# Kernel optimization log

Hardware: AMD Instinct MI355X
Metric: run time of the kernel (lower is better)

The kernel has to match this reference:

```python
import jax, jax.numpy as jnp
import numpy as np

LN_EPS = 1e-5


def layer_norm(x, w, b):
    mu = jnp.mean(x, axis=-1, keepdims=True)
    var = jnp.mean(jnp.square(x - mu), axis=-1, keepdims=True)
    return (x - mu) * jax.lax.rsqrt(var + LN_EPS) * w + b


def setup_inputs() -> dict:
    key = jax.random.key(0)
    ks = jax.random.split(key, 10)
    B, S, D, H, DH, F = 2, 2048, 1024, 16, 64, 4096

    def xavier(k, shape):
        fan_in, fan_out = shape[-1], int(np.prod(shape[:-1]))
        lim = float(np.sqrt(6.0 / (fan_in + fan_out)))
        return jax.random.uniform(k, shape, jnp.float32, -lim, lim)

    x = jax.random.normal(ks[0], (B, S, D), jnp.float32)
    W_Q = xavier(ks[1], (H, DH, D))
    W_K = xavier(ks[2], (H, DH, D))
    W_V = xavier(ks[3], (H, DH, D))
    W_O = xavier(ks[4], (D, DH, H))
    mlp_w1 = jax.random.normal(ks[5], (F, D), jnp.float32) * (1.0 / np.sqrt(D))
    mlp_b1 = jnp.zeros((F,), jnp.float32)
    mlp_w2 = jax.random.normal(ks[6], (D, F), jnp.float32) * (1.0 / np.sqrt(F))
    mlp_b2 = jnp.zeros((D,), jnp.float32)
    ln_att_w = jnp.ones((D,), jnp.float32)
    ln_att_b = jnp.zeros((D,), jnp.float32)
    ln_mlp_w = jnp.ones((D,), jnp.float32)
    ln_mlp_b = jnp.zeros((D,), jnp.float32)
    return dict(x=x, W_Q=W_Q, W_K=W_K, W_V=W_V, W_O=W_O,
                ln_att_w=ln_att_w, ln_att_b=ln_att_b,
                ln_mlp_w=ln_mlp_w, ln_mlp_b=ln_mlp_b,
                mlp_w1=mlp_w1, mlp_b1=mlp_b1, mlp_w2=mlp_w2, mlp_b2=mlp_b2)


def reference(x, W_Q, W_K, W_V, W_O, ln_att_w, ln_att_b, ln_mlp_w, ln_mlp_b,
              mlp_w1, mlp_b1, mlp_w2, mlp_b2):
    B, S, D = x.shape
    d_head = W_Q.shape[1]
    y = layer_norm(x, ln_att_w, ln_att_b)
    Q = jnp.einsum('ihd,bpd->biph', W_Q, y)  # [B,H,S,dh]
    K = jnp.einsum('ihd,bpd->biph', W_K, y)
    V = jnp.einsum('ihd,bpd->biph', W_V, y)
    scores = jnp.einsum('biph,biqh->biqp', K, Q)  # [B,H,q,p]
    causal = jnp.tril(jnp.ones((S, S), jnp.bool_))  # True where attended
    masked = scores - 1e10 * (~causal).astype(scores.dtype)
    att = jax.nn.softmax(masked / np.sqrt(d_head), axis=-1)
    z = jnp.einsum('biph,biqp->biqh', V, att)
    x_att = jnp.einsum('dhi,biqh->bqd', W_O, z)
    x = x + x_att
    y2 = layer_norm(x, ln_mlp_w, ln_mlp_b)
    h = jax.nn.relu(y2 @ mlp_w1.T + mlp_b1)
    x = x + (h @ mlp_w2.T + mlp_b2)
    return x, att
```

## Files before the change

### kernel.cpp

```cpp
#include <hip/hip_runtime.h>
#include <hip/hip_bf16.h>
#include <stdint.h>

typedef __attribute__((ext_vector_type(8))) short bf16x8;
typedef __attribute__((ext_vector_type(4))) short short4v;
typedef __attribute__((ext_vector_type(4))) float f32x4;

#define GLOAD16(g, s) __builtin_amdgcn_global_load_lds( \
    (const __attribute__((address_space(1))) void*)(g),  \
    (__attribute__((address_space(3))) void*)(s), 16, 0, 0)

static __device__ __forceinline__ short f2bf(float f) {
  unsigned u = __builtin_bit_cast(unsigned, f);
  u += 0x7fffu + ((u >> 16) & 1u);
  return (short)(u >> 16);
}

static __device__ __forceinline__ f32x4 mfma16(bf16x8 a, bf16x8 b, f32x4 c) {
  return __builtin_amdgcn_mfma_f32_16x16x32_bf16(a, b, c, 0, 0, 0);
}

template <int MODE, int BM, int BN>
static __device__ __forceinline__ void gemm_body(
    int lid, int nbx,
    const short* __restrict__ A, const short* __restrict__ Bw,
    float* __restrict__ outF, short* __restrict__ outB,
    const float* __restrict__ resid, const float* __restrict__ bias,
    int M, int N, int K, short* As, short* Bs) {
  constexpr int RBM = BM / 2, RBN = BN / 2;
  constexpr int FM = RBM / 16, FN = RBN / 16;
  constexpr int TCA = BM / 8, TCB = BN / 8, TC = TCA + TCB;
  const int tid = threadIdx.x, lane = tid & 63, wave = tid >> 6;
  const int m0 = (lid / nbx) * BM, n0 = (lid % nbx) * BN;
  const int wm = (wave & 1) * RBM, wn = (wave >> 1) * RBN;
  const int lr = lane >> 3;
  const int lc = (lane & 7) * 8;
  f32x4 acc[FM][FN] = {};

  for (int kt = 0; kt < K; kt += 64) {
#pragma unroll
    for (int i = 0; i < TC / 4; ++i) {
      const int ch = i * 4 + wave;
      if (ch < TCA) {
        GLOAD16(A + (size_t)(m0 + ch * 8 + lr) * K + kt + lc, &As[ch * 512]);
      } else {
        const int cb = ch - TCA;
        GLOAD16(Bw + (size_t)(n0 + cb * 8 + lr) * K + kt + lc, &Bs[cb * 512]);
      }
    }
    __syncthreads();
#pragma unroll
    for (int kk = 0; kk < 64; kk += 32) {
      bf16x8 af[FM], bfr[FN];
#pragma unroll
      for (int i2 = 0; i2 < FM; ++i2)
        af[i2] = *(const bf16x8*)&As[(wm + i2 * 16 + (lane & 15)) * 64 + kk + (lane >> 4) * 8];
#pragma unroll
      for (int j2 = 0; j2 < FN; ++j2)
        bfr[j2] = *(const bf16x8*)&Bs[(wn + j2 * 16 + (lane & 15)) * 64 + kk + (lane >> 4) * 8];
#pragma unroll
      for (int i2 = 0; i2 < FM; ++i2)
#pragma unroll
        for (int j2 = 0; j2 < FN; ++j2)
          acc[i2][j2] = mfma16(af[i2], bfr[j2], acc[i2][j2]);
    }
    __syncthreads();
  }

#pragma unroll
  for (int i2 = 0; i2 < FM; ++i2)
#pragma unroll
    for (int j2 = 0; j2 < FN; ++j2)
#pragma unroll
      for (int r = 0; r < 4; ++r) {
        const int m = m0 + wm + i2 * 16 + (lane >> 4) * 4 + r;
        const int n = n0 + wn + j2 * 16 + (lane & 15);
        const float v = acc[i2][j2][r];
        if (MODE == 0) {
          const size_t oi = (size_t)(n >> 10) * 4194304 +
              ((size_t)((m >> 11) * 16 + ((n & 1023) >> 6)) * 2048 + (m & 2047)) * 64 +
              (n & 63);
          outB[oi] = f2bf(v);
        } else if (MODE == 1) {
          outF[(size_t)m * N + n] = resid[(size_t)m * N + n] + v;
        } else if (MODE == 2) {
          const float t2 = v + bias[n];
          outB[(size_t)m * N + n] = f2bf(t2 > 0.0f ? t2 : 0.0f);
        } else {
          outF[(size_t)m * N + n] = resid[(size_t)m * N + n] + v + bias[n];
        }
      }
}

template <int MODE, int BM, int BN>
__global__ __launch_bounds__(256) void gemm_bf16k(
    const short* __restrict__ A, const short* __restrict__ Bw,
    float* __restrict__ outF, short* __restrict__ outB,
    const float* __restrict__ resid, const float* __restrict__ bias,
    int M, int N, int K) {
  __shared__ short As[BM * 64];
  __shared__ short Bs[BN * 64];
  const int nbx = gridDim.x, nwg = nbx * gridDim.y;
  int lid = (int)blockIdx.y * nbx + (int)blockIdx.x;
  lid = (lid & 7) * (nwg >> 3) + (lid >> 3);
  gemm_body<MODE, BM, BN>(lid, nbx, A, Bw, outF, outB, resid, bias, M, N, K, As, Bs);
}

__global__ __launch_bounds__(256) void prep_all(
    const float* __restrict__ WQ, const float* __restrict__ WK,
    const float* __restrict__ WV, const float* __restrict__ WO,
    const float* __restrict__ w1, const float* __restrict__ w2,
    const float* __restrict__ x, const float* __restrict__ lnw,
    const float* __restrict__ lnb,
    short* __restrict__ Wqkv, short* __restrict__ Wob,
    short* __restrict__ w1b, short* __restrict__ w2b,
    short* __restrict__ yb) {
  __shared__ float red[8];
  const int bi = blockIdx.x, tid = threadIdx.x;
  if (bi < 3072) {
    const float* src = bi < 1024 ? WQ : (bi < 2048 ? WK : WV);
    const float4 v = ((const float4*)(src + (size_t)(bi & 1023) * 1024))[tid];
    short4v o;
    o[0] = f2bf(v.x); o[1] = f2bf(v.y); o[2] = f2bf(v.z); o[3] = f2bf(v.w);
    ((short4v*)(Wqkv + (size_t)bi * 1024))[tid] = o;
  } else if (bi < 7168) {
    const int i = (bi - 3072) * 256 + tid;
    const float4 v = ((const float4*)w1)[i];
    short4v o;
    o[0] = f2bf(v.x); o[1] = f2bf(v.y); o[2] = f2bf(v.z); o[3] = f2bf(v.w);
    ((short4v*)w1b)[i] = o;
  } else if (bi < 11264) {
    const int i = (bi - 7168) * 256 + tid;
    const float4 v = ((const float4*)w2)[i];
    short4v o;
    o[0] = f2bf(v.x); o[1] = f2bf(v.y); o[2] = f2bf(v.z); o[3] = f2bf(v.w);
    ((short4v*)w2b)[i] = o;
  } else if (bi < 15360) {
    const int idx = (bi - 11264) * 256 + tid;
    const int d = idx >> 10, cc = idx & 1023;
    const int i = cc >> 6, h = cc & 63;
    Wob[idx] = f2bf(WO[((size_t)d * 64 + h) * 16 + i]);
  } else {
    const int row = bi - 15360;
    const int lane = tid & 63, wave = tid >> 6;
    const float4 xv = *(const float4*)&x[(size_t)row * 1024 + tid * 4];
    float s1 = xv.x + xv.y + xv.z + xv.w;
    float s2 = xv.x * xv.x + xv.y * xv.y + xv.z * xv.z + xv.w * xv.w;
#pragma unroll
    for (int off = 1; off < 64; off <<= 1) {
      s1 += __shfl_xor(s1, off);
      s2 += __shfl_xor(s2, off);
    }
    if (lane == 0) { red[wave] = s1; red[4 + wave] = s2; }
    __syncthreads();
    s1 = red[0] + red[1] + red[2] + red[3];
    s2 = red[4] + red[5] + red[6] + red[7];
    const float mu = s1 * (1.0f / 1024.0f);
    const float var = s2 * (1.0f / 1024.0f) - mu * mu;
    const float rs = rsqrtf(var + 1e-5f);
    const float4 wv = *(const float4*)&lnw[tid * 4];
    const float4 bv = *(const float4*)&lnb[tid * 4];
    short4v o;
    o[0] = f2bf((xv.x - mu) * rs * wv.x + bv.x);
    o[1] = f2bf((xv.y - mu) * rs * wv.y + bv.y);
    o[2] = f2bf((xv.z - mu) * rs * wv.z + bv.z);
    o[3] = f2bf((xv.w - mu) * rs * wv.w + bv.w);
    *(short4v*)&yb[(size_t)row * 1024 + tid * 4] = o;
  }
}

__global__ __launch_bounds__(256) void ln_kernel(const float* __restrict__ x,
                                                 const float* __restrict__ w,
                                                 const float* __restrict__ b,
                                                 short* __restrict__ y) {
  const int row = blockIdx.x, tid = threadIdx.x;
  const int lane = tid & 63, wave = tid >> 6;
  const float4 xv = *(const float4*)&x[(size_t)row * 1024 + tid * 4];
  float s1 = xv.x + xv.y + xv.z + xv.w;
  float s2 = xv.x * xv.x + xv.y * xv.y + xv.z * xv.z + xv.w * xv.w;
#pragma unroll
  for (int off = 1; off < 64; off <<= 1) {
    s1 += __shfl_xor(s1, off);
    s2 += __shfl_xor(s2, off);
  }
  __shared__ float red[8];
  if (lane == 0) { red[wave] = s1; red[4 + wave] = s2; }
  __syncthreads();
  s1 = red[0] + red[1] + red[2] + red[3];
  s2 = red[4] + red[5] + red[6] + red[7];
  const float mu = s1 * (1.0f / 1024.0f);
  const float var = s2 * (1.0f / 1024.0f) - mu * mu;
  const float rs = rsqrtf(var + 1e-5f);
  const float4 wv = *(const float4*)&w[tid * 4];
  const float4 bv = *(const float4*)&b[tid * 4];
  short4v o;
  o[0] = f2bf((xv.x - mu) * rs * wv.x + bv.x);
  o[1] = f2bf((xv.y - mu) * rs * wv.y + bv.y);
  o[2] = f2bf((xv.z - mu) * rs * wv.z + bv.z);
  o[3] = f2bf((xv.w - mu) * rs * wv.w + bv.w);
  *(short4v*)&y[(size_t)row * 1024 + tid * 4] = o;
}

__global__ __launch_bounds__(256) void transpose_v(const short* __restrict__ V,
                                                   short* __restrict__ Vt) {
  __shared__ short t[64][72];
  const int bi = blockIdx.y;
  const int p0 = blockIdx.x * 64;
  const short* Vh = V + (size_t)bi * 2048 * 64;
  short* Vth = Vt + (size_t)bi * 64 * 2048;
  const int tid = threadIdx.x;
  {
    const int pr = tid >> 2, h0 = (tid & 3) * 16;
    const bf16x8* src = (const bf16x8*)&Vh[(size_t)(p0 + pr) * 64 + h0];
    bf16x8 v0 = src[0], v1 = src[1];
#pragma unroll
    for (int j = 0; j < 8; ++j) { t[pr][h0 + j] = v0[j]; t[pr][h0 + 8 + j] = v1[j]; }
  }
  __syncthreads();
  {
    const int hr = tid >> 2, pq = (tid & 3) * 16;
    bf16x8 o0, o1;
#pragma unroll
    for (int j = 0; j < 8; ++j) { o0[j] = t[pq + j][hr]; o1[j] = t[pq + 8 + j][hr]; }
    *(bf16x8*)&Vth[(size_t)hr * 2048 + p0 + pq] = o0;
    *(bf16x8*)&Vth[(size_t)hr * 2048 + p0 + pq + 8] = o1;
  }
}

__global__ __launch_bounds__(256, 2) void attn_flash(
    const short* __restrict__ Q, const short* __restrict__ K,
    const short* __restrict__ Vt, float* __restrict__ ml,
    short* __restrict__ zb) {
  __shared__ __align__(16) char smem[34816];
  const int tid = threadIdx.x, lane = tid & 63, pc = tid >> 6;
  const int g = lane >> 4, c = lane & 15;
  const int qt = 63 - (int)blockIdx.x;
  const int bi = blockIdx.y;
  const int b = bi >> 4, hd = bi & 15;
  const size_t hoff = (size_t)bi * 2048 * 64;
  const short* Qh = Q + hoff;
  const short* Kh = K + hoff;
  const short* Vth = Vt + hoff;
  short* zbh = zb + (size_t)b * 2048 * 1024 + hd * 64;

  const int qw = qt * 32;
  const int P = qw + 32;
  const int csz = ((P + 511) >> 9) << 7;
  const int p_lo = pc * csz;
  const int p_hi = min(p_lo + csz, P);

  short* pbuf = (short*)smem + pc * 4224;
  float* mlb  = (float*)(smem + 33792);
  float* zm   = (float*)smem;

  const bf16x8* qp0 = (const bf16x8*)&Qh[(size_t)(qw + c) * 64];
  const bf16x8* qp1 = (const bf16x8*)&Qh[(size_t)(qw + 16 + c) * 64];
  bf16x8 aq[2][2];
  aq[0][0] = qp0[g]; aq[0][1] = qp0[4 + g];
  aq[1][0] = qp1[g]; aq[1][1] = qp1[4 + g];

  float m4[2][4], l4[2][4];
  f32x4 zacc[2][4] = {};
#pragma unroll
  for (int rb = 0; rb < 2; ++rb)
#pragma unroll
    for (int r = 0; r < 4; ++r) { m4[rb][r] = -1e30f; l4[rb][r] = 0.0f; }

  for (int p0 = p_lo; p0 < p_hi; p0 += 128) {
    bf16x8 k0[8], k1[8];
#pragma unroll
    for (int kb = 0; kb < 8; ++kb) {
      int row = p0 + kb * 16 + c;
      row = row < 2047 ? row : 2047;
      const bf16x8* kp = (const bf16x8*)&Kh[(size_t)row * 64];
      k0[kb] = kp[g]; k1[kb] = kp[4 + g];
    }
    const bool needmask = (p0 + 128 > qw);
#pragma unroll
    for (int rb = 0; rb < 2; ++rb) {
      f32x4 s[8];
#pragma unroll
      for (int kb = 0; kb < 8; ++kb) {
        f32x4 z4 = {0.0f, 0.0f, 0.0f, 0.0f};
        z4 = mfma16(aq[rb][0], k0[kb], z4);
        s[kb] = mfma16(aq[rb][1], k1[kb], z4);
      }
#pragma unroll
      for (int r = 0; r < 4; ++r) {
        const int q = qw + rb * 16 + g * 4 + r;
        float v[8];
        if (needmask) {
#pragma unroll
          for (int kb = 0; kb < 8; ++kb)
            v[kb] = (p0 + kb * 16 + c <= q) ? s[kb][r] * 0.125f : -1e30f;
        } else {
#pragma unroll
          for (int kb = 0; kb < 8; ++kb) v[kb] = s[kb][r] * 0.125f;
        }
        float mx = fmaxf(fmaxf(fmaxf(v[0], v[1]), fmaxf(v[2], v[3])),
                         fmaxf(fmaxf(v[4], v[5]), fmaxf(v[6], v[7])));
#pragma unroll
        for (int off = 1; off < 16; off <<= 1)
          mx = fmaxf(mx, __shfl_xor(mx, off));
        const float mn = fmaxf(m4[rb][r], mx);
        const float fac = __expf(m4[rb][r] - mn);
        m4[rb][r] = mn;
        float lsum = 0.0f;
        if (needmask) {
#pragma unroll
          for (int kb = 0; kb < 8; ++kb) {
            const int p = p0 + kb * 16 + c;
            const float e = (p <= q) ? __expf(v[kb] - mn) : 0.0f;
            lsum += e;
            pbuf[(rb * 16 + g * 4 + r) * 132 + kb * 16 + c] = f2bf(e);
          }
        } else {
#pragma unroll
          for (int kb = 0; kb < 8; ++kb) {
            const float e = __expf(v[kb] - mn);
            lsum += e;
            pbuf[(rb * 16 + g * 4 + r) * 132 + kb * 16 + c] = f2bf(e);
          }
        }
        l4[rb][r] = l4[rb][r] * fac + lsum;
#pragma unroll
        for (int hb = 0; hb < 4; ++hb) zacc[rb][hb][r] *= fac;
      }
    }
#pragma unroll
    for (int j = 0; j < 4; ++j) {
      const short4v p0lo = *(const short4v*)&pbuf[c * 132 + j * 32 + g * 8];
      const short4v p0hi = *(const short4v*)&pbuf[c * 132 + j * 32 + g * 8 + 4];
      const short4v p1lo = *(const short4v*)&pbuf[(16 + c) * 132 + j * 32 + g * 8];
      const short4v p1hi = *(const short4v*)&pbuf[(16 + c) * 132 + j * 32 + g * 8 + 4];
      const bf16x8 pa0 = __builtin_shufflevector(p0lo, p0hi, 0, 1, 2, 3, 4, 5, 6, 7);
      const bf16x8 pa1 = __builtin_shufflevector(p1lo, p1hi, 0, 1, 2, 3, 4, 5, 6, 7);
#pragma unroll
      for (int hb = 0; hb < 4; ++hb) {
        const bf16x8 bv =
            *(const bf16x8*)&Vth[(size_t)(hb * 16 + c) * 2048 + p0 + j * 32 + g * 8];
        zacc[0][hb] = mfma16(pa0, bv, zacc[0][hb]);
        zacc[1][hb] = mfma16(pa1, bv, zacc[1][hb]);
      }
    }
  }

#pragma unroll
  for (int rb = 0; rb < 2; ++rb)
#pragma unroll
    for (int r = 0; r < 4; ++r)
#pragma unroll
      for (int off = 1; off < 16; off <<= 1)
        l4[rb][r] += __shfl_xor(l4[rb][r], off);

  if (c == 0) {
#pragma unroll
    for (int rb = 0; rb < 2; ++rb)
#pragma unroll
      for (int r = 0; r < 4; ++r) {
        mlb[(pc * 32 + rb * 16 + g * 4 + r) * 2 + 0] = m4[rb][r];
        mlb[(pc * 32 + rb * 16 + g * 4 + r) * 2 + 1] = l4[rb][r];
      }
  }
  __syncthreads();

  if (pc != 0) {
#pragma unroll
    for (int rb = 0; rb < 2; ++rb)
#pragma unroll
      for (int hb = 0; hb < 4; ++hb)
#pragma unroll
        for (int r = 0; r < 4; ++r)
          zm[((pc - 1) * 32 + rb * 16 + g * 4 + r) * 68 + hb * 16 + c] = zacc[rb][hb][r];
  }
  __syncthreads();
  if (pc == 0) {
#pragma unroll
    for (int rb = 0; rb < 2; ++rb)
#pragma unroll
      for (int r = 0; r < 4; ++r) {
        const int row = rb * 16 + g * 4 + r;
        float M = -1e30f;
#pragma unroll
        for (int j = 0; j < 4; ++j) M = fmaxf(M, mlb[(j * 32 + row) * 2 + 0]);
        float w[4], L = 0.0f;
#pragma unroll
        for (int j = 0; j < 4; ++j) {
          w[j] = __expf(mlb[(j * 32 + row) * 2 + 0] - M);
          L += mlb[(j * 32 + row) * 2 + 1] * w[j];
        }
        const float iL = 1.0f / L;
#pragma unroll
        for (int hb = 0; hb < 4; ++hb) {
          float z = zacc[rb][hb][r] * w[0];
#pragma unroll
          for (int j = 1; j < 4; ++j)
            z += zm[((j - 1) * 32 + row) * 68 + hb * 16 + c] * w[j];
          zbh[(size_t)(qw + row) * 1024 + hb * 16 + c] = f2bf(z * iL);
        }
        if (c == 0)
          ((float2*)ml)[(size_t)bi * 2048 + qw + row] = make_float2(M, iL);
      }
  }
}

__global__ __launch_bounds__(256) void fused_wo_attw(
    const short* __restrict__ zbuf, const short* __restrict__ Wob,
    float* __restrict__ x1, const float* __restrict__ x,
    const short* __restrict__ Q, const short* __restrict__ K,
    const float* __restrict__ ml, float* __restrict__ att) {
  __shared__ __align__(16) char sm[24576];
  if (blockIdx.x < 512) {
    gemm_body<1, 128, 64>((int)blockIdx.x, 16, zbuf, Wob, x1, nullptr, x,
                          nullptr, 4096, 1024, 1024, (short*)sm,
                          (short*)sm + 128 * 64);
    return;
  }
  const int id = (int)blockIdx.x - 512;
  const int bi = id >> 9;
  const int rem = id & 511;
  const int qt = rem >> 3, pt = rem & 7;
  const int tid = threadIdx.x, lane = tid & 63, wave = tid >> 6;
  const int g = lane >> 4, c = lane & 15;
  const int qs = wave >> 1, ph = wave & 1;
  const int qw = qt * 32 + qs * 16;
  const int pb = pt * 256 + ph * 128;
  float* atth = att + (size_t)bi * 2048 * 2048;
  const int r0 = lane >> 3, c4 = (lane & 7) * 4;

  if (pb > qw + 15) {
    const f32x4 zf = {0.0f, 0.0f, 0.0f, 0.0f};
#pragma unroll
    for (int j = 0; j < 4; ++j) {
      __builtin_nontemporal_store(zf, (f32x4*)&atth[(size_t)(qw + r0) * 2048 + pb + j * 32 + c4]);
      __builtin_nontemporal_store(zf, (f32x4*)&atth[(size_t)(qw + 8 + r0) * 2048 + pb + j * 32 + c4]);
    }
    return;
  }

  const size_t hoff = (size_t)bi * 2048 * 64;
  const short* Qh = Q + hoff;
  const short* Kh = K + hoff;
  const bf16x8* qp = (const bf16x8*)&Qh[(size_t)(qw + c) * 64];
  const bf16x8 aq0 = qp[g], aq1 = qp[4 + g];
  float m4[4], il[4];
#pragma unroll
  for (int r = 0; r < 4; ++r) {
    const float2 t = ((const float2*)ml)[(size_t)bi * 2048 + qw + g * 4 + r];
    m4[r] = t.x; il[r] = t.y;
  }
  float* fbuf = (float*)sm + wave * 576;
  for (int p0 = pb; p0 < pb + 128; p0 += 32) {
    const bf16x8* kp0 = (const bf16x8*)&Kh[(size_t)(p0 + c) * 64];
    const bf16x8* kp1 = (const bf16x8*)&Kh[(size_t)(p0 + 16 + c) * 64];
    f32x4 s0 = {0.0f, 0.0f, 0.0f, 0.0f}, s1 = {0.0f, 0.0f, 0.0f, 0.0f};
    s0 = mfma16(aq0, kp0[g], s0);
    s0 = mfma16(aq1, kp0[4 + g], s0);
    s1 = mfma16(aq0, kp1[g], s1);
    s1 = mfma16(aq1, kp1[4 + g], s1);
#pragma unroll
    for (int f = 0; f < 2; ++f) {
      const f32x4& ss = f ? s1 : s0;
#pragma unroll
      for (int r = 0; r < 4; ++r) {
        const int q = qw + g * 4 + r, p = p0 + f * 16 + c;
        const float e = (p <= q) ? __expf(ss[r] * 0.125f - m4[r]) * il[r] : 0.0f;
        fbuf[(g * 4 + r) * 36 + f * 16 + c] = e;
      }
    }
    const f32x4 v0 = *(const f32x4*)&fbuf[r0 * 36 + c4];
    const f32x4 v1 = *(const f32x4*)&fbuf[(8 + r0) * 36 + c4];
    __builtin_nontemporal_store(v0, (f32x4*)&atth[(size_t)(qw + r0) * 2048 + p0 + c4]);
    __builtin_nontemporal_store(v1, (f32x4*)&atth[(size_t)(qw + 8 + r0) * 2048 + p0 + c4]);
  }
}

extern "C" void kernel_launch(void* const* d_in, const int* in_sizes, int n_in,
                              void* d_out, int out_size, void* d_ws, size_t ws_size,
                              hipStream_t stream) {
  (void)in_sizes; (void)n_in; (void)out_size; (void)ws_size;
  const float* x    = (const float*)d_in[0];
  const float* WQ   = (const float*)d_in[1];
  const float* WK   = (const float*)d_in[2];
  const float* WV   = (const float*)d_in[3];
  const float* WO   = (const float*)d_in[4];
  const float* lnaw = (const float*)d_in[5];
  const float* lnab = (const float*)d_in[6];
  const float* lnmw = (const float*)d_in[7];
  const float* lnmb = (const float*)d_in[8];
  const float* w1   = (const float*)d_in[9];
  const float* b1   = (const float*)d_in[10];
  const float* w2   = (const float*)d_in[11];
  const float* b2   = (const float*)d_in[12];

  char* ws = (char*)d_ws;
  const size_t MB = 1024 * 1024;
  short* Wqkv = (short*)(ws + 0 * MB);
  short* Wob  = (short*)(ws + 6 * MB);
  short* w1b  = (short*)(ws + 8 * MB);
  short* w2b  = (short*)(ws + 16 * MB);
  short* yb   = (short*)(ws + 24 * MB);
  short* Qb   = (short*)(ws + 32 * MB);
  short* Kb   = (short*)(ws + 40 * MB);
  short* Vb   = (short*)(ws + 48 * MB);
  short* Vtb  = (short*)(ws + 56 * MB);
  short* zbuf = (short*)(ws + 64 * MB);
  float* x1   = (float*)(ws + 72 * MB);
  float* mlw  = (float*)(ws + 88 * MB);
  short* hb   = (short*)(ws + 32 * MB);

  float* outx = (float*)d_out;
  float* att  = outx + (size_t)2 * 2048 * 1024;

  prep_all<<<dim3(19456), dim3(256), 0, stream>>>(
      WQ, WK, WV, WO, w1, w2, x, lnaw, lnab, Wqkv, Wob, w1b, w2b, yb);

  gemm_bf16k<0, 128, 128><<<dim3(24, 32), dim3(256), 0, stream>>>(
      yb, Wqkv, nullptr, Qb, nullptr, nullptr, 4096, 3072, 1024);

  transpose_v<<<dim3(32, 32), dim3(256), 0, stream>>>(Vb, Vtb);

  attn_flash<<<dim3(64, 32), dim3(256), 0, stream>>>(Qb, Kb, Vtb, mlw, zbuf);

  fused_wo_attw<<<dim3(16896), dim3(256), 0, stream>>>(
      zbuf, Wob, x1, x, Qb, Kb, mlw, att);

  ln_kernel<<<dim3(4096), dim3(256), 0, stream>>>(x1, lnmw, lnmb, yb);

  gemm_bf16k<2, 128, 128><<<dim3(32, 32), dim3(256), 0, stream>>>(
      yb, w1b, nullptr, hb, nullptr, b1, 4096, 4096, 1024);
  gemm_bf16k<3, 128, 64><<<dim3(16, 32), dim3(256), 0, stream>>>(
      hb, w2b, outx, nullptr, x1, b2, 4096, 1024, 4096);
}
```

Baseline: 493.1 us.

## Split fused Wo-GEMM/attention-write kernel and add MFMA priority hints in flash attention

The combined kernel that ran the Wo projection GEMM and the attention-probability write in one grid is split into two launches: a dedicated att_write kernel with a 3D grid, followed by a separate Wo GEMM launch. The GEMM body is folded back into the kernel template. The m/l statistics buffer is moved to alias the x1 region, which is safe because att_write consumes it before the GEMM writes x1. s_setprio hints are also added around the MFMA sections of attn_flash so waves in their matrix phase get issue priority. The split gives up the overlap of the GEMM with the memory-bound attention writes, in exchange for simpler scheduling and smaller LDS use per kernel.

```diff
diff --git a/kernel.cpp b/kernel.cpp
--- a/kernel.cpp
+++ b/kernel.cpp
@@ -18,92 +18,6 @@
 
 static __device__ __forceinline__ f32x4 mfma16(bf16x8 a, bf16x8 b, f32x4 c) {
   return __builtin_amdgcn_mfma_f32_16x16x32_bf16(a, b, c, 0, 0, 0);
-}
-
-template <int MODE, int BM, int BN>
-static __device__ __forceinline__ void gemm_body(
-    int lid, int nbx,
-    const short* __restrict__ A, const short* __restrict__ Bw,
-    float* __restrict__ outF, short* __restrict__ outB,
-    const float* __restrict__ resid, const float* __restrict__ bias,
-    int M, int N, int K, short* As, short* Bs) {
-  constexpr int RBM = BM / 2, RBN = BN / 2;
-  constexpr int FM = RBM / 16, FN = RBN / 16;
-  constexpr int TCA = BM / 8, TCB = BN / 8, TC = TCA + TCB;
-  const int tid = threadIdx.x, lane = tid & 63, wave = tid >> 6;
-  const int m0 = (lid / nbx) * BM, n0 = (lid % nbx) * BN;
-  const int wm = (wave & 1) * RBM, wn = (wave >> 1) * RBN;
-  const int lr = lane >> 3;
-  const int lc = (lane & 7) * 8;
-  f32x4 acc[FM][FN] = {};
-
-  for (int kt = 0; kt < K; kt += 64) {
-#pragma unroll
-    for (int i = 0; i < TC / 4; ++i) {
-      const int ch = i * 4 + wave;
-      if (ch < TCA) {
-        GLOAD16(A + (size_t)(m0 + ch * 8 + lr) * K + kt + lc, &As[ch * 512]);
-      } else {
-        const int cb = ch - TCA;
-        GLOAD16(Bw + (size_t)(n0 + cb * 8 + lr) * K + kt + lc, &Bs[cb * 512]);
-      }
-    }
-    __syncthreads();
-#pragma unroll
-    for (int kk = 0; kk < 64; kk += 32) {
-      bf16x8 af[FM], bfr[FN];
-#pragma unroll
-      for (int i2 = 0; i2 < FM; ++i2)
-        af[i2] = *(const bf16x8*)&As[(wm + i2 * 16 + (lane & 15)) * 64 + kk + (lane >> 4) * 8];
-#pragma unroll
-      for (int j2 = 0; j2 < FN; ++j2)
-        bfr[j2] = *(const bf16x8*)&Bs[(wn + j2 * 16 + (lane & 15)) * 64 + kk + (lane >> 4) * 8];
-#pragma unroll
-      for (int i2 = 0; i2 < FM; ++i2)
-#pragma unroll
-        for (int j2 = 0; j2 < FN; ++j2)
-          acc[i2][j2] = mfma16(af[i2], bfr[j2], acc[i2][j2]);
-    }
-    __syncthreads();
-  }
-
-#pragma unroll
-  for (int i2 = 0; i2 < FM; ++i2)
-#pragma unroll
-    for (int j2 = 0; j2 < FN; ++j2)
-#pragma unroll
-      for (int r = 0; r < 4; ++r) {
-        const int m = m0 + wm + i2 * 16 + (lane >> 4) * 4 + r;
-        const int n = n0 + wn + j2 * 16 + (lane & 15);
-        const float v = acc[i2][j2][r];
-        if (MODE == 0) {
-          const size_t oi = (size_t)(n >> 10) * 4194304 +
-              ((size_t)((m >> 11) * 16 + ((n & 1023) >> 6)) * 2048 + (m & 2047)) * 64 +
-              (n & 63);
-          outB[oi] = f2bf(v);
-        } else if (MODE == 1) {
-          outF[(size_t)m * N + n] = resid[(size_t)m * N + n] + v;
-        } else if (MODE == 2) {
-          const float t2 = v + bias[n];
-          outB[(size_t)m * N + n] = f2bf(t2 > 0.0f ? t2 : 0.0f);
-        } else {
-          outF[(size_t)m * N + n] = resid[(size_t)m * N + n] + v + bias[n];
-        }
-      }
-}
-
-template <int MODE, int BM, int BN>
-__global__ __launch_bounds__(256) void gemm_bf16k(
-    const short* __restrict__ A, const short* __restrict__ Bw,
-    float* __restrict__ outF, short* __restrict__ outB,
-    const float* __restrict__ resid, const float* __restrict__ bias,
-    int M, int N, int K) {
-  __shared__ short As[BM * 64];
-  __shared__ short Bs[BN * 64];
-  const int nbx = gridDim.x, nwg = nbx * gridDim.y;
-  int lid = (int)blockIdx.y * nbx + (int)blockIdx.x;
-  lid = (lid & 7) * (nwg >> 3) + (lid >> 3);
-  gemm_body<MODE, BM, BN>(lid, nbx, A, Bw, outF, outB, resid, bias, M, N, K, As, Bs);
 }
 
 __global__ __launch_bounds__(256) void prep_all(
@@ -201,6 +115,82 @@
   *(short4v*)&y[(size_t)row * 1024 + tid * 4] = o;
 }
 
+template <int MODE, int BM, int BN>
+__global__ __launch_bounds__(256) void gemm_bf16k(
+    const short* __restrict__ A, const short* __restrict__ Bw,
+    float* __restrict__ outF, short* __restrict__ outB,
+    const float* __restrict__ resid, const float* __restrict__ bias,
+    int M, int N, int K) {
+  constexpr int RBM = BM / 2, RBN = BN / 2;
+  constexpr int FM = RBM / 16, FN = RBN / 16;
+  constexpr int TCA = BM / 8, TCB = BN / 8, TC = TCA + TCB;
+  __shared__ short As[BM * 64];
+  __shared__ short Bs[BN * 64];
+  const int tid = threadIdx.x, lane = tid & 63, wave = tid >> 6;
+  const int nbx = gridDim.x, nwg = nbx * gridDim.y;
+  int lid = (int)blockIdx.y * nbx + (int)blockIdx.x;
+  lid = (lid & 7) * (nwg >> 3) + (lid >> 3);
+  const int m0 = (lid / nbx) * BM, n0 = (lid % nbx) * BN;
+  const int wm = (wave & 1) * RBM, wn = (wave >> 1) * RBN;
+  const int lr = lane >> 3;
+  const int lc = (lane & 7) * 8;
+  f32x4 acc[FM][FN] = {};
+
+  for (int kt = 0; kt < K; kt += 64) {
+#pragma unroll
+    for (int i = 0; i < TC / 4; ++i) {
+      const int ch = i * 4 + wave;
+      if (ch < TCA) {
+        GLOAD16(A + (size_t)(m0 + ch * 8 + lr) * K + kt + lc, &As[ch * 512]);
+      } else {
+        const int cb = ch - TCA;
+        GLOAD16(Bw + (size_t)(n0 + cb * 8 + lr) * K + kt + lc, &Bs[cb * 512]);
+      }
+    }
+    __syncthreads();
+#pragma unroll
+    for (int kk = 0; kk < 64; kk += 32) {
+      bf16x8 af[FM], bfr[FN];
+#pragma unroll
+      for (int i2 = 0; i2 < FM; ++i2)
+        af[i2] = *(const bf16x8*)&As[(wm + i2 * 16 + (lane & 15)) * 64 + kk + (lane >> 4) * 8];
+#pragma unroll
+      for (int j2 = 0; j2 < FN; ++j2)
+        bfr[j2] = *(const bf16x8*)&Bs[(wn + j2 * 16 + (lane & 15)) * 64 + kk + (lane >> 4) * 8];
+#pragma unroll
+      for (int i2 = 0; i2 < FM; ++i2)
+#pragma unroll
+        for (int j2 = 0; j2 < FN; ++j2)
+          acc[i2][j2] = mfma16(af[i2], bfr[j2], acc[i2][j2]);
+    }
+    __syncthreads();
+  }
+
+#pragma unroll
+  for (int i2 = 0; i2 < FM; ++i2)
+#pragma unroll
+    for (int j2 = 0; j2 < FN; ++j2)
+#pragma unroll
+      for (int r = 0; r < 4; ++r) {
+        const int m = m0 + wm + i2 * 16 + (lane >> 4) * 4 + r;
+        const int n = n0 + wn + j2 * 16 + (lane & 15);
+        const float v = acc[i2][j2][r];
+        if (MODE == 0) {
+          const size_t oi = (size_t)(n >> 10) * 4194304 +
+              ((size_t)((m >> 11) * 16 + ((n & 1023) >> 6)) * 2048 + (m & 2047)) * 64 +
+              (n & 63);
+          outB[oi] = f2bf(v);
+        } else if (MODE == 1) {
+          outF[(size_t)m * N + n] = resid[(size_t)m * N + n] + v;
+        } else if (MODE == 2) {
+          const float t2 = v + bias[n];
+          outB[(size_t)m * N + n] = f2bf(t2 > 0.0f ? t2 : 0.0f);
+        } else {
+          outF[(size_t)m * N + n] = resid[(size_t)m * N + n] + v + bias[n];
+        }
+      }
+}
+
 __global__ __launch_bounds__(256) void transpose_v(const short* __restrict__ V,
                                                    short* __restrict__ Vt) {
   __shared__ short t[64][72];
@@ -279,12 +269,14 @@
 #pragma unroll
     for (int rb = 0; rb < 2; ++rb) {
       f32x4 s[8];
+      __builtin_amdgcn_s_setprio(1);
 #pragma unroll
       for (int kb = 0; kb < 8; ++kb) {
         f32x4 z4 = {0.0f, 0.0f, 0.0f, 0.0f};
         z4 = mfma16(aq[rb][0], k0[kb], z4);
         s[kb] = mfma16(aq[rb][1], k1[kb], z4);
       }
+      __builtin_amdgcn_s_setprio(0);
 #pragma unroll
       for (int r = 0; r < 4; ++r) {
         const int q = qw + rb * 16 + g * 4 + r;
@@ -327,6 +319,7 @@
         for (int hb = 0; hb < 4; ++hb) zacc[rb][hb][r] *= fac;
       }
     }
+    __builtin_amdgcn_s_setprio(1);
 #pragma unroll
     for (int j = 0; j < 4; ++j) {
       const short4v p0lo = *(const short4v*)&pbuf[c * 132 + j * 32 + g * 8];
@@ -343,6 +336,7 @@
         zacc[1][hb] = mfma16(pa1, bv, zacc[1][hb]);
       }
     }
+    __builtin_amdgcn_s_setprio(0);
   }
 
 #pragma unroll
@@ -404,24 +398,13 @@
   }
 }
 
-__global__ __launch_bounds__(256) void fused_wo_attw(
-    const short* __restrict__ zbuf, const short* __restrict__ Wob,
-    float* __restrict__ x1, const float* __restrict__ x,
+__global__ __launch_bounds__(256) void att_write(
     const short* __restrict__ Q, const short* __restrict__ K,
     const float* __restrict__ ml, float* __restrict__ att) {
-  __shared__ __align__(16) char sm[24576];
-  if (blockIdx.x < 512) {
-    gemm_body<1, 128, 64>((int)blockIdx.x, 16, zbuf, Wob, x1, nullptr, x,
-                          nullptr, 4096, 1024, 1024, (short*)sm,
-                          (short*)sm + 128 * 64);
-    return;
-  }
-  const int id = (int)blockIdx.x - 512;
-  const int bi = id >> 9;
-  const int rem = id & 511;
-  const int qt = rem >> 3, pt = rem & 7;
+  __shared__ float fbuf_s[4][16 * 36];
   const int tid = threadIdx.x, lane = tid & 63, wave = tid >> 6;
   const int g = lane >> 4, c = lane & 15;
+  const int qt = blockIdx.x, pt = blockIdx.y, bi = blockIdx.z;
   const int qs = wave >> 1, ph = wave & 1;
   const int qw = qt * 32 + qs * 16;
   const int pb = pt * 256 + ph * 128;
@@ -449,7 +432,7 @@
     const float2 t = ((const float2*)ml)[(size_t)bi * 2048 + qw + g * 4 + r];
     m4[r] = t.x; il[r] = t.y;
   }
-  float* fbuf = (float*)sm + wave * 576;
+  float* fbuf = fbuf_s[wave];
   for (int p0 = pb; p0 < pb + 128; p0 += 32) {
     const bf16x8* kp0 = (const bf16x8*)&Kh[(size_t)(p0 + c) * 64];
     const bf16x8* kp1 = (const bf16x8*)&Kh[(size_t)(p0 + 16 + c) * 64];
@@ -506,7 +489,7 @@
   short* Vtb  = (short*)(ws + 56 * MB);
   short* zbuf = (short*)(ws + 64 * MB);
   float* x1   = (float*)(ws + 72 * MB);
-  float* mlw  = (float*)(ws + 88 * MB);
+  float* mlw  = (float*)(ws + 72 * MB);
   short* hb   = (short*)(ws + 32 * MB);
 
   float* outx = (float*)d_out;
@@ -522,8 +505,10 @@
 
   attn_flash<<<dim3(64, 32), dim3(256), 0, stream>>>(Qb, Kb, Vtb, mlw, zbuf);
 
-  fused_wo_attw<<<dim3(16896), dim3(256), 0, stream>>>(
-      zbuf, Wob, x1, x, Qb, Kb, mlw, att);
+  att_write<<<dim3(64, 8, 32), dim3(256), 0, stream>>>(Qb, Kb, mlw, att);
+
+  gemm_bf16k<1, 128, 64><<<dim3(16, 32), dim3(256), 0, stream>>>(
+      zbuf, Wob, x1, nullptr, x, nullptr, 4096, 1024, 1024);
 
   ln_kernel<<<dim3(4096), dim3(256), 0, stream>>>(x1, lnmw, lnmb, yb);
 
```

Result: faster. 464.9 us (-5.7%).
